# Optimization experiments

Measured on AMD Instinct MI355X. Metric: run time of the kernel, lower is better.

## Reference

```python
import jax, jax.numpy as jnp
import numpy as np

INPUT_WIDTH = 256
DEPTH = 7
OUTPUT_WIDTH = 256
N_NODES = 2 ** (DEPTH + 1) - 1  # 255


def setup_inputs() -> dict:
    key = jax.random.key(0)
    k_x, k_w1, k_w2 = jax.random.split(key, 3)
    init1 = 1.0 / np.sqrt(INPUT_WIDTH)
    x = jax.random.normal(k_x, (2, 1024, INPUT_WIDTH), dtype=jnp.float32)
    w1s = jax.random.uniform(k_w1, (N_NODES, INPUT_WIDTH), jnp.float32, -init1, init1)
    b1s = jnp.zeros((N_NODES,), jnp.float32)
    w2s = jax.random.uniform(k_w2, (N_NODES, INPUT_WIDTH, OUTPUT_WIDTH), jnp.float32, -init1, init1)
    b2s = jnp.zeros((N_NODES, OUTPUT_WIDTH), jnp.float32)
    return {"x": x, "w1s": w1s, "b1s": b1s, "w2s": w2s, "b2s": b2s}


def reference(x, w1s, b1s, w2s, b2s):
    B, S, D = x.shape
    flat_x = x.reshape(B * S, D)  # [T, D]
    T = flat_x.shape[0]

    # --- routing pass: walk the binary tree, recording node ids and logits ---
    current = jnp.zeros((T,), dtype=jnp.int32)
    all_nodes = []
    all_logits = []
    for _ in range(DEPTH + 1):
        all_nodes.append(current)
        score = jnp.einsum('td,td->t', flat_x, w1s[current]) + b1s[current]  # [T]
        all_logits.append(score)
        # ((sign+1)/2).long(): sign(0)->0 maps to choice 0 via truncation
        choice = ((jnp.sign(score) + 1.0) / 2.0).astype(jnp.int32)
        current = current * 2 + choice + 1

    logits = jnp.stack(all_logits, axis=1)  # [T, DEPTH+1]
    path_weights = jax.nn.gelu(jnp.abs(logits), approximate=False)  # exact erf GELU

    # --- output pass: weighted sum of per-node transforms along the path ---
    out = jnp.zeros((T, OUTPUT_WIDTH), dtype=x.dtype)
    for i in range(DEPTH + 1):
        nodes_i = all_nodes[i]
        t_i = jnp.einsum('td,tdo->to', flat_x, w2s[nodes_i]) + b2s[nodes_i]  # [T, O]
        out = out + t_i * path_weights[:, i][:, None]

    return out.reshape(B, S, OUTPUT_WIDTH)
```

## Files before the change

kernel.cpp:

```cpp
#include <hip/hip_runtime.h>
#include <hip/hip_bf16.h>

#define T_TOKENS 2048
#define DIM 256
#define NLEV 8

using bf16x8 = __attribute__((ext_vector_type(8))) short;
using f32x4  = __attribute__((ext_vector_type(4))) float;

__device__ __forceinline__ unsigned short f2bf(float f) {
    union { float f; unsigned u; } v; v.f = f;
    unsigned r = v.u + 0x7FFFu + ((v.u >> 16) & 1u);
    return (unsigned short)(r >> 16);
}

__global__ __launch_bounds__(256) void route_kernel(
    const float* __restrict__ x, const float* __restrict__ w1s,
    const float* __restrict__ b1s,
    float* __restrict__ pw,
    int*   __restrict__ pc)
{
    int wave = threadIdx.x >> 6;
    int lane = threadIdx.x & 63;
    int t = blockIdx.x * 4 + wave;

    const float4 xv = *reinterpret_cast<const float4*>(x + (size_t)t * DIM + lane * 4);
    int p = 1;
    float keep = 0.0f;
    #pragma unroll
    for (int lvl = 0; lvl < NLEV; ++lvl) {
        int node = p - 1;
        const float4 wv = *reinterpret_cast<const float4*>(w1s + (size_t)node * DIM + lane * 4);
        float s = xv.x * wv.x + xv.y * wv.y + xv.z * wv.z + xv.w * wv.w;
        #pragma unroll
        for (int off = 32; off; off >>= 1) s += __shfl_xor(s, off);
        float score = s + b1s[node];
        float a = fabsf(score);
        float g = a * 0.5f * (1.0f + erff(a * 0.70710678118654752f));
        if (lane == lvl) keep = g;
        int choice = (score > 0.0f) ? 1 : 0;
        p = 2 * p + choice;
    }
    if (lane < NLEV) pw[(size_t)t * NLEV + lane] = keep;
    if (lane == 0) pc[t] = p;
}

__global__ __launch_bounds__(256) void sort_kernel(
    const int* __restrict__ pc,
    int* __restrict__ order, unsigned* __restrict__ units, int* __restrict__ ucount)
{
    __shared__ int hist[256];
    __shared__ int offs[256];
    __shared__ int cums[257];
    __shared__ int wpart[4];
    int tid = threadIdx.x;
    hist[tid] = 0;
    __syncthreads();

    int myPc[8];
    #pragma unroll
    for (int i = 0; i < 8; ++i) {
        int t = tid * 8 + i;
        myPc[i] = pc[t];
        atomicAdd(&hist[myPc[i] - 256], 1);
    }
    __syncthreads();

    if (tid < 64) {
        int lane = tid;
        int v0 = hist[lane * 4 + 0], v1 = hist[lane * 4 + 1];
        int v2 = hist[lane * 4 + 2], v3 = hist[lane * 4 + 3];
        int sum = v0 + v1 + v2 + v3;
        int scan = sum;
        #pragma unroll
        for (int off = 1; off < 64; off <<= 1) {
            int n = __shfl_up(scan, off);
            if (lane >= off) scan += n;
        }
        int excl = scan - sum;
        offs[lane * 4 + 0] = excl;
        offs[lane * 4 + 1] = excl + v0;
        offs[lane * 4 + 2] = excl + v0 + v1;
        offs[lane * 4 + 3] = excl + v0 + v1 + v2;
    }
    __syncthreads();

    cums[tid] = offs[tid];
    if (tid == 0) cums[256] = T_TOKENS;
    __syncthreads();

    #pragma unroll
    for (int i = 0; i < 8; ++i) {
        int t = tid * 8 + i;
        int bin = myPc[i] - 256;
        int pos = atomicAdd(&offs[bin], 1);
        order[pos] = t;
    }

    int nch = 0, s = 0, e = 0, l = 0;
    if (tid < 255) {
        int q = tid + 1;
        l = 31 - __clz(q);
        int shift = 8 - l;
        int lo = (q << shift) - 256;
        int hi = ((q + 1) << shift) - 256;
        s = cums[lo];
        e = cums[hi];
        nch = (e - s + 63) >> 6;
    }
    int lane = tid & 63, w = tid >> 6;
    int scan = nch;
    #pragma unroll
    for (int off = 1; off < 64; off <<= 1) {
        int n = __shfl_up(scan, off);
        if (lane >= off) scan += n;
    }
    if (lane == 63) wpart[w] = scan;
    __syncthreads();
    int pre = 0;
    for (int k = 0; k < w; ++k) pre += wpart[k];
    int base = pre + scan - nch;
    for (int j = 0; j < nch; ++j) {
        int st = s + j * 64;
        int c = e - st; if (c > 64) c = 64;
        units[base + j] = (unsigned)tid | ((unsigned)l << 8) |
                          ((unsigned)st << 11) | ((unsigned)c << 22);
    }
    if (tid == 255) *ucount = pre + scan;
}

__global__ __launch_bounds__(256, 2) void out_kernel(
    const float* __restrict__ x, const float* __restrict__ w2s,
    const float* __restrict__ b2s, const float* __restrict__ pw,
    const int* __restrict__ order, const unsigned* __restrict__ units,
    const int* __restrict__ ucount, float* __restrict__ out)
{
    __shared__ unsigned short As[16384];
    __shared__ unsigned short Bs[2][8192];

    int u = blockIdx.x;
    if (u >= *ucount) return;
    unsigned d = units[u];
    int node  = (int)(d & 255u);
    int lvl   = (int)((d >> 8) & 7u);
    int start = (int)((d >> 11) & 2047u);
    int cnt   = (int)((d >> 22) & 127u);

    int tid = threadIdx.x;
    int wv = tid >> 6, lane = tid & 63;
    int l15 = lane & 15, kg = lane >> 4;

    const float* w2n = w2s + ((size_t)node << 16);

    float La[32];
    auto loadB = [&](int p) {
        const float* bp = w2n + (size_t)(p * 32 + wv * 8) * DIM + lane * 4;
        #pragma unroll
        for (int j = 0; j < 8; ++j) {
            float4 v = *reinterpret_cast<const float4*>(bp + (size_t)j * DIM);
            La[j * 4 + 0] = v.x; La[j * 4 + 1] = v.y;
            La[j * 4 + 2] = v.z; La[j * 4 + 3] = v.w;
        }
    };
    auto writeB = [&](unsigned short* bs) {
        #pragma unroll
        for (int q = 0; q < 4; ++q) {
            bf16x8 v;
            #pragma unroll
            for (int j = 0; j < 8; ++j) v[j] = (short)f2bf(La[j * 4 + q]);
            int col = lane * 4 + q;
            int g = wv * 256 + (col ^ ((col >> 3) & 7));
            *reinterpret_cast<bf16x8*>(&bs[g * 8]) = v;
        }
    };

    loadB(0);

    {
        int r = tid >> 2, seg = tid & 3;
        if (r < cnt) {
            int t = order[start + r];
            const float* xp = x + (size_t)t * DIM + seg * 64;
            #pragma unroll
            for (int g = 0; g < 8; ++g) {
                float4 a0 = *reinterpret_cast<const float4*>(xp + g * 8);
                float4 a1 = *reinterpret_cast<const float4*>(xp + g * 8 + 4);
                bf16x8 v;
                v[0] = (short)f2bf(a0.x); v[1] = (short)f2bf(a0.y);
                v[2] = (short)f2bf(a0.z); v[3] = (short)f2bf(a0.w);
                v[4] = (short)f2bf(a1.x); v[5] = (short)f2bf(a1.y);
                v[6] = (short)f2bf(a1.z); v[7] = (short)f2bf(a1.w);
                int gk = seg * 8 + g;
                int gg = r * 32 + (gk ^ (r & 7));
                *reinterpret_cast<bf16x8*>(&As[gg * 8]) = v;
            }
        }
    }
    writeB(Bs[0]);
    __syncthreads();

    f32x4 acc[4][4];
    #pragma unroll
    for (int m = 0; m < 4; ++m)
        #pragma unroll
        for (int nb = 0; nb < 4; ++nb) acc[m][nb] = (f32x4){0.f, 0.f, 0.f, 0.f};

    for (int p = 0; p < 8; ++p) {
        if (p < 7) loadB(p + 1);
        unsigned short* bs = Bs[p & 1];
        bf16x8 a[4], b[4];
        #pragma unroll
        for (int m = 0; m < 4; ++m) if (m * 16 < cnt) {
            int row = m * 16 + l15;
            int g = row * 32 + ((p * 4 + kg) ^ (row & 7));
            a[m] = *reinterpret_cast<bf16x8*>(&As[g * 8]);
        }
        #pragma unroll
        for (int nb = 0; nb < 4; ++nb) {
            int col = wv * 64 + nb * 16 + l15;
            int g = kg * 256 + (col ^ ((col >> 3) & 7));
            b[nb] = *reinterpret_cast<bf16x8*>(&bs[g * 8]);
        }
        #pragma unroll
        for (int m = 0; m < 4; ++m) if (m * 16 < cnt)
            #pragma unroll
            for (int nb = 0; nb < 4; ++nb)
                acc[m][nb] = __builtin_amdgcn_mfma_f32_16x16x32_bf16(a[m], b[nb], acc[m][nb], 0, 0, 0);
        if (p < 7) writeB(Bs[(p + 1) & 1]);
        __syncthreads();
    }

    float bias[4];
    #pragma unroll
    for (int nb = 0; nb < 4; ++nb)
        bias[nb] = b2s[((size_t)node << 8) + wv * 64 + nb * 16 + l15];

    #pragma unroll
    for (int m = 0; m < 4; ++m) if (m * 16 < cnt) {
        #pragma unroll
        for (int j = 0; j < 4; ++j) {
            int r = m * 16 + kg * 4 + j;
            if (r < cnt) {
                int t = order[start + r];
                float w = pw[(size_t)t * NLEV + lvl];
                #pragma unroll
                for (int nb = 0; nb < 4; ++nb) {
                    float val = w * (acc[m][nb][j] + bias[nb]);
                    atomicAdd(&out[(size_t)t * DIM + wv * 64 + nb * 16 + l15], val);
                }
            }
        }
    }
}

extern "C" void kernel_launch(void* const* d_in, const int* in_sizes, int n_in,
                              void* d_out, int out_size, void* d_ws, size_t ws_size,
                              hipStream_t stream) {
    const float* x   = (const float*)d_in[0];
    const float* w1s = (const float*)d_in[1];
    const float* b1s = (const float*)d_in[2];
    const float* w2s = (const float*)d_in[3];
    const float* b2s = (const float*)d_in[4];
    float* out = (float*)d_out;

    float* pw       = (float*)d_ws;
    int* pc         = (int*)(pw + T_TOKENS * NLEV);
    int* order      = pc + T_TOKENS;
    unsigned* units = (unsigned*)(order + T_TOKENS);
    int* ucount     = (int*)(units + 512);

    hipMemsetAsync(d_out, 0, (size_t)out_size * sizeof(float), stream);
    route_kernel<<<T_TOKENS / 4, 256, 0, stream>>>(x, w1s, b1s, pw, pc);
    sort_kernel<<<1, 256, 0, stream>>>(pc, order, units, ucount);
    out_kernel<<<512, 256, 0, stream>>>(x, w2s, b2s, pw, order, units, ucount, out);
}
```

Before: 52.54 us.

## Split output columns across two blocks per unit and deepen weight prefetch

Each work unit (node, level, token chunk) is now handled by two blocks, each covering half of the 256 output columns. The grid doubles, the B tile in shared memory halves, and occupancy is raised to 3 blocks per CU. Weight loads are prefetched two stages ahead through two register buffers so global-load latency overlaps more of the MFMA work. The goal is more parallelism and better latency hiding on the memory-bound weight stream. The cost is that the shared x tile is loaded and converted twice per unit, and each load is a narrower float2.

```diff
diff --git a/kernel.cpp b/kernel.cpp
--- a/kernel.cpp
+++ b/kernel.cpp
@@ -129,16 +129,17 @@
     if (tid == 255) *ucount = pre + scan;
 }
 
-__global__ __launch_bounds__(256, 2) void out_kernel(
+__global__ __launch_bounds__(256, 3) void out_kernel(
     const float* __restrict__ x, const float* __restrict__ w2s,
     const float* __restrict__ b2s, const float* __restrict__ pw,
     const int* __restrict__ order, const unsigned* __restrict__ units,
     const int* __restrict__ ucount, float* __restrict__ out)
 {
     __shared__ unsigned short As[16384];
-    __shared__ unsigned short Bs[2][8192];
-
-    int u = blockIdx.x;
+    __shared__ unsigned short Bs[2][4096];
+
+    int u = blockIdx.x >> 1;
+    int ch = blockIdx.x & 1;
     if (u >= *ucount) return;
     unsigned d = units[u];
     int node  = (int)(d & 255u);
@@ -150,31 +151,30 @@
     int wv = tid >> 6, lane = tid & 63;
     int l15 = lane & 15, kg = lane >> 4;
 
-    const float* w2n = w2s + ((size_t)node << 16);
-
-    float La[32];
-    auto loadB = [&](int p) {
-        const float* bp = w2n + (size_t)(p * 32 + wv * 8) * DIM + lane * 4;
+    const float* w2n = w2s + ((size_t)node << 16) + ch * 128;
+
+    float2 La0[8], La1[8];
+    auto loadB = [&](int p, float2 (&La)[8]) {
+        const float* bp = w2n + (size_t)(p * 32 + wv * 8) * DIM + lane * 2;
+        #pragma unroll
+        for (int j = 0; j < 8; ++j)
+            La[j] = *reinterpret_cast<const float2*>(bp + (size_t)j * DIM);
+    };
+    auto writeB = [&](unsigned short* bs, const float2 (&La)[8]) {
+        bf16x8 v0, v1;
         #pragma unroll
         for (int j = 0; j < 8; ++j) {
-            float4 v = *reinterpret_cast<const float4*>(bp + (size_t)j * DIM);
-            La[j * 4 + 0] = v.x; La[j * 4 + 1] = v.y;
-            La[j * 4 + 2] = v.z; La[j * 4 + 3] = v.w;
-        }
+            v0[j] = (short)f2bf(La[j].x);
+            v1[j] = (short)f2bf(La[j].y);
+        }
+        int g0 = wv * 128 + lane * 2;
+        int g1 = g0 + 1;
+        *reinterpret_cast<bf16x8*>(&bs[(g0 ^ ((g0 >> 3) & 7)) * 8]) = v0;
+        *reinterpret_cast<bf16x8*>(&bs[(g1 ^ ((g1 >> 3) & 7)) * 8]) = v1;
     };
-    auto writeB = [&](unsigned short* bs) {
-        #pragma unroll
-        for (int q = 0; q < 4; ++q) {
-            bf16x8 v;
-            #pragma unroll
-            for (int j = 0; j < 8; ++j) v[j] = (short)f2bf(La[j * 4 + q]);
-            int col = lane * 4 + q;
-            int g = wv * 256 + (col ^ ((col >> 3) & 7));
-            *reinterpret_cast<bf16x8*>(&bs[g * 8]) = v;
-        }
-    };
-
-    loadB(0);
+
+    loadB(0, La0);
+    loadB(1, La1);
 
     {
         int r = tid >> 2, seg = tid & 3;
@@ -196,19 +196,27 @@
             }
         }
     }
-    writeB(Bs[0]);
-    __syncthreads();
-
-    f32x4 acc[4][4];
+    writeB(Bs[0], La0);
+    __syncthreads();
+
+    f32x4 acc[4][2];
     #pragma unroll
     for (int m = 0; m < 4; ++m)
         #pragma unroll
-        for (int nb = 0; nb < 4; ++nb) acc[m][nb] = (f32x4){0.f, 0.f, 0.f, 0.f};
-
+        for (int nb = 0; nb < 2; ++nb) acc[m][nb] = (f32x4){0.f, 0.f, 0.f, 0.f};
+
+    #pragma unroll
     for (int p = 0; p < 8; ++p) {
-        if (p < 7) loadB(p + 1);
+        if (p < 6) {
+            if (p & 1) loadB(p + 2, La1); else loadB(p + 2, La0);
+        }
         unsigned short* bs = Bs[p & 1];
-        bf16x8 a[4], b[4];
+        bf16x8 a[4], b[2];
+        #pragma unroll
+        for (int nb = 0; nb < 2; ++nb) {
+            int g = kg * 128 + wv * 32 + nb * 16 + l15;
+            b[nb] = *reinterpret_cast<bf16x8*>(&bs[(g ^ ((g >> 3) & 7)) * 8]);
+        }
         #pragma unroll
         for (int m = 0; m < 4; ++m) if (m * 16 < cnt) {
             int row = m * 16 + l15;
@@ -216,24 +224,20 @@
             a[m] = *reinterpret_cast<bf16x8*>(&As[g * 8]);
         }
         #pragma unroll
-        for (int nb = 0; nb < 4; ++nb) {
-            int col = wv * 64 + nb * 16 + l15;
-            int g = kg * 256 + (col ^ ((col >> 3) & 7));
-            b[nb] = *reinterpret_cast<bf16x8*>(&bs[g * 8]);
-        }
-        #pragma unroll
         for (int m = 0; m < 4; ++m) if (m * 16 < cnt)
             #pragma unroll
-            for (int nb = 0; nb < 4; ++nb)
+            for (int nb = 0; nb < 2; ++nb)
                 acc[m][nb] = __builtin_amdgcn_mfma_f32_16x16x32_bf16(a[m], b[nb], acc[m][nb], 0, 0, 0);
-        if (p < 7) writeB(Bs[(p + 1) & 1]);
+        if (p < 7) {
+            if (p & 1) writeB(Bs[(p + 1) & 1], La0); else writeB(Bs[(p + 1) & 1], La1);
+        }
         __syncthreads();
     }
 
-    float bias[4];
-    #pragma unroll
-    for (int nb = 0; nb < 4; ++nb)
-        bias[nb] = b2s[((size_t)node << 8) + wv * 64 + nb * 16 + l15];
+    float bias[2];
+    #pragma unroll
+    for (int nb = 0; nb < 2; ++nb)
+        bias[nb] = b2s[((size_t)node << 8) + ch * 128 + wv * 32 + nb * 16 + l15];
 
     #pragma unroll
     for (int m = 0; m < 4; ++m) if (m * 16 < cnt) {
@@ -244,9 +248,9 @@
                 int t = order[start + r];
                 float w = pw[(size_t)t * NLEV + lvl];
                 #pragma unroll
-                for (int nb = 0; nb < 4; ++nb) {
+                for (int nb = 0; nb < 2; ++nb) {
                     float val = w * (acc[m][nb][j] + bias[nb]);
-                    atomicAdd(&out[(size_t)t * DIM + wv * 64 + nb * 16 + l15], val);
+                    atomicAdd(&out[(size_t)t * DIM + ch * 128 + wv * 32 + nb * 16 + l15], val);
                 }
             }
         }
@@ -272,5 +276,5 @@
     hipMemsetAsync(d_out, 0, (size_t)out_size * sizeof(float), stream);
     route_kernel<<<T_TOKENS / 4, 256, 0, stream>>>(x, w1s, b1s, pw, pc);
     sort_kernel<<<1, 256, 0, stream>>>(pc, order, units, ucount);
-    out_kernel<<<512, 256, 0, stream>>>(x, w2s, b2s, pw, order, units, ucount, out);
-}
+    out_kernel<<<1024, 256, 0, stream>>>(x, w2s, b2s, pw, order, units, ucount, out);
+}
```

Result: no change. 52.45 us (-0.2%).
